# Optimization experiments

Measured on AMD Instinct MI355X. Metric: run time of the kernel, lower is better.

## Reference

```python
import jax, jax.numpy as jnp
import numpy as np

B, T, D, H = 2, 2048, 1024, 16
HS = D // H
EPS = 1e-5


def setup_inputs() -> dict:
    key = jax.random.key(0)
    ks = jax.random.split(key, 16)
    s = lambda *shape: 0.02
    inp = {
        "x": jax.random.normal(ks[0], (B, T, D), jnp.float32),
        # per-head Q/K/V weights stacked over heads: [H, D, HS]
        "Wq": jax.random.normal(ks[1], (H, D, HS), jnp.float32) * 0.02,
        "bq": jnp.zeros((H, HS), jnp.float32),
        "Wk": jax.random.normal(ks[2], (H, D, HS), jnp.float32) * 0.02,
        "bk": jnp.zeros((H, HS), jnp.float32),
        "Wv": jax.random.normal(ks[3], (H, D, HS), jnp.float32) * 0.02,
        "bv": jnp.zeros((H, HS), jnp.float32),
        "Wp": jax.random.normal(ks[4], (D, D), jnp.float32) * 0.02,
        "bp": jnp.zeros((D,), jnp.float32),
        "W1": jax.random.normal(ks[5], (D, 4 * D), jnp.float32) * 0.02,
        "b1": jnp.zeros((4 * D,), jnp.float32),
        "W2": jax.random.normal(ks[6], (4 * D, D), jnp.float32) * 0.02,
        "b2": jnp.zeros((D,), jnp.float32),
        "g1": jnp.ones((D,), jnp.float32),
        "be1": jnp.zeros((D,), jnp.float32),
        "g2": jnp.ones((D,), jnp.float32),
        "be2": jnp.zeros((D,), jnp.float32),
    }
    return inp


def layernorm(x, g, b):
    mu = jnp.mean(x, axis=-1, keepdims=True)
    var = jnp.mean(jnp.square(x - mu), axis=-1, keepdims=True)
    return (x - mu) * jax.lax.rsqrt(var + EPS) * g + b


def reference(x, Wq, bq, Wk, bk, Wv, bv, Wp, bp, W1, b1, W2, b2, g1, be1, g2, be2):
    # NOTE: this block applies LN then residual-adds the *normalized* x,
    # exactly as in the original (x = ln1(x); x = x + mha(x)).
    h = layernorm(x, g1, be1)
    # multi-head attention, all heads batched via stacked weights
    q = jnp.einsum('btd,hdk->bhtk', h, Wq) + bq[None, :, None, :]
    k = jnp.einsum('btd,hdk->bhtk', h, Wk) + bk[None, :, None, :]
    v = jnp.einsum('btd,hdk->bhtk', h, Wv) + bv[None, :, None, :]
    att = jnp.einsum('bhtk,bhsk->bhts', q, k) * (HS ** -0.5)  # [B,H,T,T]
    att = jax.nn.softmax(att, axis=-1)
    o = jnp.einsum('bhts,bhsk->bhtk', att, v)  # [B,H,T,HS]
    # concat heads in order along last dim -> [B,T,D]
    o = jnp.transpose(o, (0, 2, 1, 3)).reshape(B, T, D)
    o = o @ Wp + bp
    h = h + o
    h2 = layernorm(h, g2, be2)
    ff = jax.nn.gelu(h2 @ W1 + b1, approximate=False) @ W2 + b2
    return h2 + ff
```

## Files before the change

### kernel.cpp

```cpp
#include <hip/hip_runtime.h>
#include <cstdint>
#include <cstddef>

#define B_  2
#define T_  2048
#define D_  1024
#define H_  16
#define HS_ 64
#define MTOT (B_*T_)

typedef unsigned short u16;
typedef __attribute__((ext_vector_type(8))) __bf16 bf16x8;
typedef __attribute__((ext_vector_type(4))) float f32x4;

__device__ __forceinline__ u16 f2bf(float f) {
  unsigned int u = __builtin_bit_cast(unsigned int, f);
  u += 0x7fffu + ((u >> 16) & 1u);
  return (u16)(u >> 16);
}

__device__ __forceinline__ unsigned cvtpk(float lo, float hi) {
  unsigned r;
  asm("v_cvt_pk_bf16_f32 %0, %1, %2" : "=v"(r) : "v"(lo), "v"(hi));
  return r;
}

__device__ __forceinline__ void gload16(const u16* g, u16* l) {
  __builtin_amdgcn_global_load_lds((const __attribute__((address_space(1))) void*)g,
                                   (__attribute__((address_space(3))) void*)l, 16, 0, 0);
}

__global__ __launch_bounds__(256) void transpose_qkv(const float* __restrict__ wq,
                                                     const float* __restrict__ wk,
                                                     const float* __restrict__ wv,
                                                     u16* __restrict__ out) {
  __shared__ float tile[32][33];
  const int R = 1024, C = 64;
  int z = blockIdx.z, sel = z >> 4, zl = z & 15;
  const float* src = (sel == 0 ? wq : (sel == 1 ? wk : wv)) + (size_t)zl * R * C;
  u16* dst = out + (size_t)sel * 1024 * 1024 + (size_t)zl * R * C;
  int c0 = blockIdx.x * 32, r0 = blockIdx.y * 32;
  int tx = threadIdx.x & 31, ty = threadIdx.x >> 5;
#pragma unroll
  for (int k = 0; k < 4; ++k)
    tile[ty + k*8][tx] = src[(size_t)(r0 + ty + k*8) * C + c0 + tx];
  __syncthreads();
#pragma unroll
  for (int k = 0; k < 4; ++k)
    dst[(size_t)(c0 + ty + k*8) * R + r0 + tx] = f2bf(tile[tx][ty + k*8]);
}

__global__ __launch_bounds__(256) void transpose_f2b(const float* __restrict__ in,
                                                     u16* __restrict__ out, int R, int C) {
  __shared__ float tile[32][33];
  int c0 = blockIdx.x * 32, r0 = blockIdx.y * 32;
  size_t zoff = (size_t)blockIdx.z * R * C;
  const float* src = in + zoff;
  u16* dst = out + zoff;
  int tx = threadIdx.x & 31, ty = threadIdx.x >> 5;
#pragma unroll
  for (int k = 0; k < 4; ++k)
    tile[ty + k*8][tx] = src[(size_t)(r0 + ty + k*8) * C + c0 + tx];
  __syncthreads();
#pragma unroll
  for (int k = 0; k < 4; ++k)
    dst[(size_t)(c0 + ty + k*8) * R + r0 + tx] = f2bf(tile[tx][ty + k*8]);
}

__global__ __launch_bounds__(256) void transpose_v(const u16* __restrict__ in,
                                                   u16* __restrict__ out) {
  __shared__ u16 tile[32][33];
  int z = blockIdx.z;
  int b = z >> 4, h = z & 15;
  int t0 = blockIdx.x * 32, f0 = blockIdx.y * 32;
  int tx = threadIdx.x & 31, ty = threadIdx.x >> 5;
#pragma unroll
  for (int k = 0; k < 4; ++k)
    tile[ty + k*8][tx] = in[((size_t)b*T_ + t0 + ty + k*8) * D_ + h*HS_ + f0 + tx];
  __syncthreads();
#pragma unroll
  for (int k = 0; k < 4; ++k)
    out[((size_t)z*HS_ + f0 + ty + k*8) * T_ + t0 + tx] = tile[tx][ty + k*8];
}

__global__ __launch_bounds__(256) void ln_kernel(const float* __restrict__ x,
                                                 const float* __restrict__ gg,
                                                 const float* __restrict__ be,
                                                 float* __restrict__ hf,
                                                 u16* __restrict__ hb) {
  int row = blockIdx.x;
  int t = threadIdx.x;
  const float* xr = x + (size_t)row * D_;
  float4 xv = *(const float4*)&xr[t * 4];
  float s  = xv.x + xv.y + xv.z + xv.w;
  float ss = xv.x*xv.x + xv.y*xv.y + xv.z*xv.z + xv.w*xv.w;
#pragma unroll
  for (int m = 1; m < 64; m <<= 1) { s += __shfl_xor(s, m); ss += __shfl_xor(ss, m); }
  __shared__ float red[8];
  int lane = t & 63, wv = t >> 6;
  if (lane == 0) { red[wv] = s; red[4 + wv] = ss; }
  __syncthreads();
  s  = red[0] + red[1] + red[2] + red[3];
  ss = red[4] + red[5] + red[6] + red[7];
  float mu  = s * (1.0f / D_);
  float var = ss * (1.0f / D_) - mu * mu;
  float rs  = rsqrtf(var + 1e-5f);
  float4 gv = *(const float4*)&gg[t * 4];
  float4 bv = *(const float4*)&be[t * 4];
  float4 hv;
  hv.x = (xv.x - mu) * rs * gv.x + bv.x;
  hv.y = (xv.y - mu) * rs * gv.y + bv.y;
  hv.z = (xv.z - mu) * rs * gv.z + bv.z;
  hv.w = (xv.w - mu) * rs * gv.w + bv.w;
  *(float4*)&hf[(size_t)row * D_ + t * 4] = hv;
  uint2 pk;
  pk.x = (unsigned)f2bf(hv.x) | ((unsigned)f2bf(hv.y) << 16);
  pk.y = (unsigned)f2bf(hv.z) | ((unsigned)f2bf(hv.w) << 16);
  *(uint2*)&hb[(size_t)row * D_ + t * 4] = pk;
}

template<int EPI>
__global__ __launch_bounds__(512, 2) void gemm256(
    const u16* __restrict__ A, const u16* __restrict__ Bt,
    const float* __restrict__ bias0, const float* __restrict__ bias1,
    const float* __restrict__ bias2,
    u16* __restrict__ o0, u16* __restrict__ o1, u16* __restrict__ o2,
    int M, int N, int K) {
  __shared__ __align__(16) u16 As[2][256 * 64];
  __shared__ __align__(16) u16 Bs[2][256 * 64];
  const int tid = threadIdx.x;
  const int lane = tid & 63, w = tid >> 6;
  const int m0 = blockIdx.y * 256, n0 = blockIdx.x * 256;
  const int rA = lane & 15, g = lane >> 4;
  const int wm = (w >> 2) * 128, wn = (w & 3) * 64;
  const int sxa = rA & 7;

  f32x4 acc[8][4] = {};

  auto stage = [&](int t, int bufi) {
#pragma unroll
    for (int i = 0; i < 4; ++i) {
      int c = i * 512 + tid;
      int row = c >> 3;
      int ss = (c & 7) ^ (row & 7);
      gload16(A + (size_t)(m0 + row) * K + t * 64 + ss * 8,
              &As[bufi][0] + (size_t)(i * 512 + w * 64) * 8);
    }
#pragma unroll
    for (int i = 0; i < 4; ++i) {
      int c = i * 512 + tid;
      int row = c >> 3;
      int ss = (c & 7) ^ (row & 7);
      gload16(Bt + (size_t)(n0 + row) * K + t * 64 + ss * 8,
              &Bs[bufi][0] + (size_t)(i * 512 + w * 64) * 8);
    }
  };

  stage(0, 0);

  const int nk = K >> 6;
  for (int t = 0; t < nk; ++t) {
    __syncthreads();
    const int buf = t & 1;
    if (t + 1 < nk) stage(t + 1, buf ^ 1);

    bf16x8 bfr[4][2];
#pragma unroll
    for (int j = 0; j < 4; ++j) {
      int br = wn + j * 16 + rA;
#pragma unroll
      for (int kk = 0; kk < 2; ++kk)
        bfr[j][kk] = *(const bf16x8*)&Bs[buf][br * 64 + (((kk * 4 + g) ^ sxa) << 3)];
    }
#pragma unroll
    for (int i = 0; i < 8; ++i) {
      int ar = wm + i * 16 + rA;
      bf16x8 a0 = *(const bf16x8*)&As[buf][ar * 64 + ((g ^ sxa) << 3)];
      bf16x8 a1 = *(const bf16x8*)&As[buf][ar * 64 + (((4 + g) ^ sxa) << 3)];
#pragma unroll
      for (int j = 0; j < 4; ++j) {
        acc[i][j] = __builtin_amdgcn_mfma_f32_16x16x32_bf16(a0, bfr[j][0], acc[i][j], 0, 0, 0);
        acc[i][j] = __builtin_amdgcn_mfma_f32_16x16x32_bf16(a1, bfr[j][1], acc[i][j], 0, 0, 0);
      }
    }
  }

#pragma unroll
  for (int i = 0; i < 8; ++i) {
#pragma unroll
    for (int j = 0; j < 4; ++j) {
#pragma unroll
      for (int r = 0; r < 4; ++r) {
        int row = m0 + wm + i * 16 + g * 4 + r;
        int col = n0 + wn + j * 16 + rA;
        float v = acc[i][j][r];
        int sel = col >> 10, nn = col & 1023;
        const float* bp = sel == 0 ? bias0 : (sel == 1 ? bias1 : bias2);
        u16* op = sel == 0 ? o0 : (sel == 1 ? o1 : o2);
        op[(size_t)row * 1024 + nn] = f2bf(v + bp[nn]);
      }
    }
  }
}

template<int EPI>
__global__ __launch_bounds__(256) void gemm_bt(
    const u16* __restrict__ A, const u16* __restrict__ Bt,
    const float* __restrict__ bias0, const float* __restrict__ res,
    float* __restrict__ outf, float* __restrict__ p1, u16* __restrict__ ob,
    int M, int N, int K, int kLen) {
  __shared__ __align__(16) u16 As[3][128 * 32];
  __shared__ __align__(16) u16 Bs[3][128 * 32];
  const int tid = threadIdx.x;
  const int lane = tid & 63, wv = tid >> 6;
  const int m0 = blockIdx.y * 128, n0 = blockIdx.x * 128;
  const int kOff = blockIdx.z * kLen;
  const int rA = lane & 15, g = lane >> 4;
  const int wm = (wv >> 1) * 64, wn = (wv & 1) * 64;
  const int sx = (rA >> 1) & 3;

  f32x4 acc[4][4] = {};

  auto stage = [&](int tt, int bufi) {
#pragma unroll
    for (int p = 0; p < 2; ++p) {
      int c = (p * 4 + wv) * 64 + lane;
      int row = c >> 2;
      int s = (c & 3) ^ ((row >> 1) & 3);
      gload16(A  + (size_t)(m0 + row) * K + kOff + tt * 32 + s * 8,
              &As[bufi][0] + (size_t)(p * 4 + wv) * 512);
      gload16(Bt + (size_t)(n0 + row) * K + kOff + tt * 32 + s * 8,
              &Bs[bufi][0] + (size_t)(p * 4 + wv) * 512);
    }
  };

  const int nk = kLen >> 5;
  stage(0, 0);
  stage(1, 1);

  int cur = 0, nxt = 2;
  for (int t = 0; t < nk; ++t) {
    if (t + 1 < nk) asm volatile("s_waitcnt vmcnt(4)" ::: "memory");
    else            asm volatile("s_waitcnt vmcnt(0)" ::: "memory");
    __builtin_amdgcn_s_barrier();
    __builtin_amdgcn_sched_barrier(0);
    if (t + 2 < nk) stage(t + 2, nxt);

    bf16x8 a[4], b[4];
#pragma unroll
    for (int i = 0; i < 4; ++i)
      a[i] = *(const bf16x8*)&As[cur][(wm + i * 16 + rA) * 32 + ((g ^ sx) << 3)];
#pragma unroll
    for (int i = 0; i < 4; ++i)
      b[i] = *(const bf16x8*)&Bs[cur][(wn + i * 16 + rA) * 32 + ((g ^ sx) << 3)];
#pragma unroll
    for (int i = 0; i < 4; ++i)
#pragma unroll
      for (int j = 0; j < 4; ++j)
        acc[i][j] = __builtin_amdgcn_mfma_f32_16x16x32_bf16(a[i], b[j], acc[i][j], 0, 0, 0);

    cur = (cur == 2) ? 0 : cur + 1;
    nxt = (nxt == 2) ? 0 : nxt + 1;
  }

#pragma unroll
  for (int i = 0; i < 4; ++i) {
#pragma unroll
    for (int j = 0; j < 4; ++j) {
#pragma unroll
      for (int r = 0; r < 4; ++r) {
        int row = m0 + wm + i * 16 + g * 4 + r;
        int col = n0 + wn + j * 16 + rA;
        float v = acc[i][j][r];
        if constexpr (EPI == 1) {
          v += bias0[col];
          float z = 0.7978845608f * (v + 0.044715f * v * v * v);
          z = fminf(z, 18.0f);
          float e = __builtin_amdgcn_exp2f(z * 2.8853900817779268f);
          v = v * e / (e + 1.0f);
          ob[(size_t)row * N + col] = f2bf(v);
        } else if constexpr (EPI == 2) {
          v += bias0[col] + res[(size_t)row * N + col];
          outf[(size_t)row * N + col] = v;
        } else {
          float* dst = blockIdx.z ? p1 : outf;
          dst[(size_t)row * N + col] = v;
        }
      }
    }
  }
}

__global__ __launch_bounds__(256) void reduce_ff2(const float* __restrict__ p0,
                                                  const float* __restrict__ p1,
                                                  const float* __restrict__ bias,
                                                  const float* __restrict__ res,
                                                  float* __restrict__ out) {
  int i = (blockIdx.x * 256 + threadIdx.x) * 4;
  float4 a = *(const float4*)&p0[i];
  float4 b = *(const float4*)&p1[i];
  float4 r = *(const float4*)&res[i];
  float4 bb = *(const float4*)&bias[i & 1023];
  float4 o;
  o.x = a.x + b.x + r.x + bb.x;
  o.y = a.y + b.y + r.y + bb.y;
  o.z = a.z + b.z + r.z + bb.z;
  o.w = a.w + b.w + r.w + bb.w;
  *(float4*)&out[i] = o;
}

__global__ __launch_bounds__(256) void attn_kernel(const u16* __restrict__ qg,
                                                   const u16* __restrict__ kg,
                                                   const u16* __restrict__ vtg,
                                                   u16* __restrict__ og) {
  const int wg = blockIdx.x;
  const int qt = wg & 31;
  const int h  = (wg >> 5) & 15;
  const int b  = wg >> 9;
  const int tid = threadIdx.x, lane = tid & 63, wv = tid >> 6;
  const int q0 = qt * 64 + wv * 16;
  const int rA = lane & 15, g = lane >> 4;
  const int rx = rA & 7;

  __shared__ __align__(16) u16 Ks[2][64 * 64];
  __shared__ __align__(16) u16 Vs[2][64 * 64];
  __shared__ __align__(16) u16 Ps[4][16 * 64];

  const size_t qoff = ((size_t)b * T_ + q0 + rA) * D_ + h * HS_ + g * 8;
  const bf16x8 aq0 = *(const bf16x8*)&qg[qoff];
  const bf16x8 aq1 = *(const bf16x8*)&qg[qoff + 32];

  const u16* kbase = kg + (size_t)b * T_ * D_ + h * HS_;
  const u16* vbase = vtg + ((size_t)b * H_ + h) * HS_ * T_;

  const float cfold = 0.18033688011112042f;
  float mrun = -1e30f, lrun = 0.0f;
  f32x4 oacc[4] = {};

  auto stage = [&](int t, int buf) {
#pragma unroll
    for (int p = 0; p < 2; ++p) {
      int chunk = p * 256 + wv * 64 + lane;
      int row = chunk >> 3, s = chunk & 7;
      int ss = s ^ (row & 7);
      gload16(kbase + ((size_t)t * 64 + row) * D_ + ss * 8,
              &Ks[buf][0] + (size_t)(p * 256 + wv * 64) * 8);
      gload16(vbase + (size_t)row * T_ + t * 64 + ss * 8,
              &Vs[buf][0] + (size_t)(p * 256 + wv * 64) * 8);
    }
  };

  stage(0, 0);

  const int NT = T_ / 64;
  for (int t = 0; t < NT; ++t) {
    __syncthreads();
    const int buf = t & 1;
    if (t + 1 < NT) stage(t + 1, buf ^ 1);

    const u16* kb = &Ks[buf][0];
    f32x4 sc[4];
    __builtin_amdgcn_s_setprio(1);
#pragma unroll
    for (int st = 0; st < 4; ++st) {
      bf16x8 k0 = *(const bf16x8*)&kb[(st * 16 + rA) * 64 + ((g ^ rx) << 3)];
      bf16x8 k1 = *(const bf16x8*)&kb[(st * 16 + rA) * 64 + (((4 + g) ^ rx) << 3)];
      f32x4 z = {};
      z = __builtin_amdgcn_mfma_f32_16x16x32_bf16(k0, aq0, z, 0, 0, 0);
      z = __builtin_amdgcn_mfma_f32_16x16x32_bf16(k1, aq1, z, 0, 0, 0);
      sc[st] = z;
    }
    __builtin_amdgcn_s_setprio(0);

    float a0 = fmaxf(fmaxf(sc[0][0], sc[0][1]), fmaxf(sc[0][2], sc[0][3]));
    float a1 = fmaxf(fmaxf(sc[1][0], sc[1][1]), fmaxf(sc[1][2], sc[1][3]));
    float a2 = fmaxf(fmaxf(sc[2][0], sc[2][1]), fmaxf(sc[2][2], sc[2][3]));
    float a3 = fmaxf(fmaxf(sc[3][0], sc[3][1]), fmaxf(sc[3][2], sc[3][3]));
    float mx = fmaxf(fmaxf(a0, a1), fmaxf(a2, a3));
    mx = fmaxf(mx, __shfl_xor(mx, 16));
    mx = fmaxf(mx, __shfl_xor(mx, 32));
    float tm = mx * cfold;

    if (__any(tm > mrun + 8.0f)) {
      float mnew = fmaxf(mrun, tm);
      float sca = __builtin_amdgcn_exp2f(mrun - mnew);
      mrun = mnew;
      lrun *= sca;
#pragma unroll
      for (int f = 0; f < 4; ++f) oacc[f] *= sca;
    }

    float p[16];
#pragma unroll
    for (int st = 0; st < 4; ++st)
#pragma unroll
      for (int r = 0; r < 4; ++r)
        p[st * 4 + r] = __builtin_amdgcn_exp2f(__builtin_fmaf(sc[st][r], cfold, -mrun));

    float sum = (((p[0] + p[1]) + (p[2] + p[3])) + ((p[4] + p[5]) + (p[6] + p[7])))
              + (((p[8] + p[9]) + (p[10] + p[11])) + ((p[12] + p[13]) + (p[14] + p[15])));
    sum += __shfl_xor(sum, 16);
    sum += __shfl_xor(sum, 32);
    lrun += sum;

    char* psb = (char*)&Ps[wv][0];
#pragma unroll
    for (int st = 0; st < 4; ++st) {
      uint2 w;
      w.x = cvtpk(p[st * 4 + 0], p[st * 4 + 1]);
      w.y = cvtpk(p[st * 4 + 2], p[st * 4 + 3]);
      int slot = st * 2 + (g >> 1);
      *(uint2*)&psb[rA * 128 + (((slot ^ rx)) << 4) + ((g & 1) << 3)] = w;
    }
    bf16x8 pf0 = *(const bf16x8*)&psb[rA * 128 + ((g ^ rx) << 4)];
    bf16x8 pf1 = *(const bf16x8*)&psb[rA * 128 + (((4 + g) ^ rx) << 4)];

    const u16* vbl = &Vs[buf][0];
    __builtin_amdgcn_s_setprio(1);
#pragma unroll
    for (int f = 0; f < 4; ++f) {
      bf16x8 v0 = *(const bf16x8*)&vbl[(f * 16 + rA) * 64 + ((g ^ rx) << 3)];
      bf16x8 v1 = *(const bf16x8*)&vbl[(f * 16 + rA) * 64 + (((4 + g) ^ rx) << 3)];
      oacc[f] = __builtin_amdgcn_mfma_f32_16x16x32_bf16(v0, pf0, oacc[f], 0, 0, 0);
      oacc[f] = __builtin_amdgcn_mfma_f32_16x16x32_bf16(v1, pf1, oacc[f], 0, 0, 0);
    }
    __builtin_amdgcn_s_setprio(0);
  }

  float linv = 1.0f / lrun;
#pragma unroll
  for (int f = 0; f < 4; ++f) {
    uint2 w;
    w.x = cvtpk(oacc[f][0] * linv, oacc[f][1] * linv);
    w.y = cvtpk(oacc[f][2] * linv, oacc[f][3] * linv);
    *(uint2*)&og[((size_t)b * T_ + q0 + rA) * D_ + h * HS_ + f * 16 + g * 4] = w;
  }
}

extern "C" void kernel_launch(void* const* d_in, const int* in_sizes, int n_in,
                              void* d_out, int out_size, void* d_ws, size_t ws_size,
                              hipStream_t stream) {
  const float* x   = (const float*)d_in[0];
  const float* Wq  = (const float*)d_in[1];
  const float* bq  = (const float*)d_in[2];
  const float* Wk  = (const float*)d_in[3];
  const float* bk  = (const float*)d_in[4];
  const float* Wv  = (const float*)d_in[5];
  const float* bv  = (const float*)d_in[6];
  const float* Wp  = (const float*)d_in[7];
  const float* bp  = (const float*)d_in[8];
  const float* W1  = (const float*)d_in[9];
  const float* b1  = (const float*)d_in[10];
  const float* W2  = (const float*)d_in[11];
  const float* b2  = (const float*)d_in[12];
  const float* g1  = (const float*)d_in[13];
  const float* be1 = (const float*)d_in[14];
  const float* g2  = (const float*)d_in[15];
  const float* be2 = (const float*)d_in[16];
  float* out = (float*)d_out;

  char* w = (char*)d_ws;
  auto alloc = [&](size_t bytes) { char* p = w; w += (bytes + 255) & ~(size_t)255; return p; };
  const size_t MD = (size_t)MTOT * D_;

  float* h_f    = (float*)alloc(MD * 4);
  u16*   h_b    = (u16*)  alloc(MD * 2);
  u16*   wqkv_t = (u16*)  alloc(3 * (size_t)D_ * D_ * 2);
  u16*   wp_t   = (u16*)  alloc((size_t)D_ * D_ * 2);
  u16*   w1_t   = (u16*)  alloc((size_t)D_ * 4 * D_ * 2);
  u16*   w2_t   = (u16*)  alloc((size_t)D_ * 4 * D_ * 2);
  u16*   q_b    = (u16*)  alloc(MD * 2);
  u16*   k_b    = (u16*)  alloc(MD * 2);
  u16*   v_b    = (u16*)  alloc(MD * 2);
  u16*   vt_b   = (u16*)  alloc(MD * 2);
  u16*   o_b    = (u16*)  alloc(MD * 2);
  float* hat_f  = (float*)alloc(MD * 4);
  u16*   ff1_b  = q_b;
  float* h2_f   = h_f;
  u16*   h2_b   = h_b;
  float* pf0    = hat_f;
  float* pf1    = (float*)h_b;

  dim3 blk(256);

  transpose_qkv<<<dim3(2, 32, 48), blk, 0, stream>>>(Wq, Wk, Wv, wqkv_t);
  transpose_f2b<<<dim3(32, 32, 1), blk, 0, stream>>>(Wp, wp_t, 1024, 1024);
  transpose_f2b<<<dim3(128, 32, 1), blk, 0, stream>>>(W1, w1_t, 1024, 4096);
  transpose_f2b<<<dim3(32, 128, 1), blk, 0, stream>>>(W2, w2_t, 4096, 1024);

  ln_kernel<<<dim3(MTOT), blk, 0, stream>>>(x, g1, be1, h_f, h_b);

  gemm256<0><<<dim3(12, 16), dim3(512), 0, stream>>>(h_b, wqkv_t, bq, bk, bv,
      q_b, k_b, v_b, MTOT, 3072, 1024);

  transpose_v<<<dim3(64, 2, 32), blk, 0, stream>>>(v_b, vt_b);

  attn_kernel<<<dim3(B_ * H_ * (T_ / 64)), blk, 0, stream>>>(q_b, k_b, vt_b, o_b);

  gemm_bt<2><<<dim3(8, 32, 1), blk, 0, stream>>>(o_b, wp_t, bp, h_f, hat_f,
      nullptr, nullptr, MTOT, 1024, 1024, 1024);

  ln_kernel<<<dim3(MTOT), blk, 0, stream>>>(hat_f, g2, be2, h2_f, h2_b);

  gemm_bt<1><<<dim3(32, 32, 1), blk, 0, stream>>>(h2_b, w1_t, b1, nullptr,
      nullptr, nullptr, ff1_b, MTOT, 4096, 1024, 1024);

  gemm_bt<3><<<dim3(8, 32, 2), blk, 0, stream>>>(ff1_b, w2_t, nullptr, nullptr,
      pf0, pf1, nullptr, MTOT, 1024, 4096, 2048);

  reduce_ff2<<<dim3(MTOT), blk, 0, stream>>>(pf0, pf1, b2, h2_f, out);
}
```

Measured before the change: 286.3 us.

## Fuse V transpose into QKV epilogue, merge weight transposes, narrow proj GEMM tile

The QKV GEMM epilogue now writes V straight into the transposed [B,H,HS,T] layout as packed bf16 pairs, so the separate transpose_v kernel and its round trip through global memory go away. The three fp32-to-bf16 weight transpose launches are merged into one kernel with a flat grid. The output-projection GEMM gets a TN template parameter and runs with 128x64 tiles, doubling its block count to 512 for better CU occupancy. The V stores are 8-byte writes strided by T, so they are less coalesced than the row-major stores.

Measured after the change: 279.6 us. -2.3%, faster.

```diff
diff --git a/kernel.cpp b/kernel.cpp
--- a/kernel.cpp
+++ b/kernel.cpp
@@ -50,13 +50,17 @@
     dst[(size_t)(c0 + ty + k*8) * R + r0 + tx] = f2bf(tile[tx][ty + k*8]);
 }
 
-__global__ __launch_bounds__(256) void transpose_f2b(const float* __restrict__ in,
-                                                     u16* __restrict__ out, int R, int C) {
+__global__ __launch_bounds__(256) void transpose_rest(
+    const float* __restrict__ Wp, const float* __restrict__ W1,
+    const float* __restrict__ W2, u16* __restrict__ wp_t,
+    u16* __restrict__ w1_t, u16* __restrict__ w2_t) {
   __shared__ float tile[32][33];
-  int c0 = blockIdx.x * 32, r0 = blockIdx.y * 32;
-  size_t zoff = (size_t)blockIdx.z * R * C;
-  const float* src = in + zoff;
-  u16* dst = out + zoff;
+  int f = blockIdx.x;
+  const float* src; u16* dst; int R, C, xx, yy;
+  if (f < 1024)      { src = Wp; dst = wp_t; R = 1024; C = 1024; xx = f & 31;  yy = f >> 5; }
+  else if (f < 5120) { int f2 = f - 1024; src = W1; dst = w1_t; R = 1024; C = 4096; xx = f2 & 127; yy = f2 >> 7; }
+  else               { int f2 = f - 5120; src = W2; dst = w2_t; R = 4096; C = 1024; xx = f2 & 31;  yy = f2 >> 5; }
+  int c0 = xx * 32, r0 = yy * 32;
   int tx = threadIdx.x & 31, ty = threadIdx.x >> 5;
 #pragma unroll
   for (int k = 0; k < 4; ++k)
@@ -65,22 +69,6 @@
 #pragma unroll
   for (int k = 0; k < 4; ++k)
     dst[(size_t)(c0 + ty + k*8) * R + r0 + tx] = f2bf(tile[tx][ty + k*8]);
-}
-
-__global__ __launch_bounds__(256) void transpose_v(const u16* __restrict__ in,
-                                                   u16* __restrict__ out) {
-  __shared__ u16 tile[32][33];
-  int z = blockIdx.z;
-  int b = z >> 4, h = z & 15;
-  int t0 = blockIdx.x * 32, f0 = blockIdx.y * 32;
-  int tx = threadIdx.x & 31, ty = threadIdx.x >> 5;
-#pragma unroll
-  for (int k = 0; k < 4; ++k)
-    tile[ty + k*8][tx] = in[((size_t)b*T_ + t0 + ty + k*8) * D_ + h*HS_ + f0 + tx];
-  __syncthreads();
-#pragma unroll
-  for (int k = 0; k < 4; ++k)
-    out[((size_t)z*HS_ + f0 + ty + k*8) * T_ + t0 + tx] = tile[tx][ty + k*8];
 }
 
 __global__ __launch_bounds__(256) void ln_kernel(const float* __restrict__ x,
@@ -189,37 +177,45 @@
   for (int i = 0; i < 8; ++i) {
 #pragma unroll
     for (int j = 0; j < 4; ++j) {
-#pragma unroll
-      for (int r = 0; r < 4; ++r) {
-        int row = m0 + wm + i * 16 + g * 4 + r;
-        int col = n0 + wn + j * 16 + rA;
-        float v = acc[i][j][r];
-        int sel = col >> 10, nn = col & 1023;
-        const float* bp = sel == 0 ? bias0 : (sel == 1 ? bias1 : bias2);
-        u16* op = sel == 0 ? o0 : (sel == 1 ? o1 : o2);
-        op[(size_t)row * 1024 + nn] = f2bf(v + bp[nn]);
+      int col = n0 + wn + j * 16 + rA;
+      int sel = col >> 10, nn = col & 1023;
+      int row0 = m0 + wm + i * 16 + g * 4;
+      if (sel == 2) {
+        float bb = bias2[nn];
+        int bb_ = row0 >> 11, t0 = row0 & 2047;
+        uint2 pkv;
+        pkv.x = cvtpk(acc[i][j][0] + bb, acc[i][j][1] + bb);
+        pkv.y = cvtpk(acc[i][j][2] + bb, acc[i][j][3] + bb);
+        *(uint2*)&o2[((size_t)(bb_ * 1024 + nn)) * 2048 + t0] = pkv;
+      } else {
+        const float* bp = sel == 0 ? bias0 : bias1;
+        u16* op = sel == 0 ? o0 : o1;
+#pragma unroll
+        for (int r = 0; r < 4; ++r)
+          op[(size_t)(row0 + r) * 1024 + nn] = f2bf(acc[i][j][r] + bp[nn]);
       }
     }
   }
 }
 
-template<int EPI>
+template<int EPI, int TN>
 __global__ __launch_bounds__(256) void gemm_bt(
     const u16* __restrict__ A, const u16* __restrict__ Bt,
     const float* __restrict__ bias0, const float* __restrict__ res,
     float* __restrict__ outf, float* __restrict__ p1, u16* __restrict__ ob,
     int M, int N, int K, int kLen) {
+  constexpr int NJ = TN / 32;
   __shared__ __align__(16) u16 As[3][128 * 32];
-  __shared__ __align__(16) u16 Bs[3][128 * 32];
+  __shared__ __align__(16) u16 Bs[3][TN * 32];
   const int tid = threadIdx.x;
   const int lane = tid & 63, wv = tid >> 6;
-  const int m0 = blockIdx.y * 128, n0 = blockIdx.x * 128;
+  const int m0 = blockIdx.y * 128, n0 = blockIdx.x * TN;
   const int kOff = blockIdx.z * kLen;
   const int rA = lane & 15, g = lane >> 4;
-  const int wm = (wv >> 1) * 64, wn = (wv & 1) * 64;
+  const int wm = (wv >> 1) * 64, wn = (wv & 1) * (TN / 2);
   const int sx = (rA >> 1) & 3;
 
-  f32x4 acc[4][4] = {};
+  f32x4 acc[4][NJ] = {};
 
   auto stage = [&](int tt, int bufi) {
 #pragma unroll
@@ -227,8 +223,14 @@
       int c = (p * 4 + wv) * 64 + lane;
       int row = c >> 2;
       int s = (c & 3) ^ ((row >> 1) & 3);
-      gload16(A  + (size_t)(m0 + row) * K + kOff + tt * 32 + s * 8,
+      gload16(A + (size_t)(m0 + row) * K + kOff + tt * 32 + s * 8,
               &As[bufi][0] + (size_t)(p * 4 + wv) * 512);
+    }
+#pragma unroll
+    for (int p = 0; p < TN / 64; ++p) {
+      int c = (p * 4 + wv) * 64 + lane;
+      int row = c >> 2;
+      int s = (c & 3) ^ ((row >> 1) & 3);
       gload16(Bt + (size_t)(n0 + row) * K + kOff + tt * 32 + s * 8,
               &Bs[bufi][0] + (size_t)(p * 4 + wv) * 512);
     }
@@ -246,17 +248,17 @@
     __builtin_amdgcn_sched_barrier(0);
     if (t + 2 < nk) stage(t + 2, nxt);
 
-    bf16x8 a[4], b[4];
+    bf16x8 a[4], b[NJ];
 #pragma unroll
     for (int i = 0; i < 4; ++i)
       a[i] = *(const bf16x8*)&As[cur][(wm + i * 16 + rA) * 32 + ((g ^ sx) << 3)];
 #pragma unroll
+    for (int j = 0; j < NJ; ++j)
+      b[j] = *(const bf16x8*)&Bs[cur][(wn + j * 16 + rA) * 32 + ((g ^ sx) << 3)];
+#pragma unroll
     for (int i = 0; i < 4; ++i)
-      b[i] = *(const bf16x8*)&Bs[cur][(wn + i * 16 + rA) * 32 + ((g ^ sx) << 3)];
-#pragma unroll
-    for (int i = 0; i < 4; ++i)
-#pragma unroll
-      for (int j = 0; j < 4; ++j)
+#pragma unroll
+      for (int j = 0; j < NJ; ++j)
         acc[i][j] = __builtin_amdgcn_mfma_f32_16x16x32_bf16(a[i], b[j], acc[i][j], 0, 0, 0);
 
     cur = (cur == 2) ? 0 : cur + 1;
@@ -266,7 +268,7 @@
 #pragma unroll
   for (int i = 0; i < 4; ++i) {
 #pragma unroll
-    for (int j = 0; j < 4; ++j) {
+    for (int j = 0; j < NJ; ++j) {
 #pragma unroll
       for (int r = 0; r < 4; ++r) {
         int row = m0 + wm + i * 16 + g * 4 + r;
@@ -480,32 +482,29 @@
   u16*   h2_b   = h_b;
   float* pf0    = hat_f;
   float* pf1    = (float*)h_b;
+  (void)v_b;
 
   dim3 blk(256);
 
   transpose_qkv<<<dim3(2, 32, 48), blk, 0, stream>>>(Wq, Wk, Wv, wqkv_t);
-  transpose_f2b<<<dim3(32, 32, 1), blk, 0, stream>>>(Wp, wp_t, 1024, 1024);
-  transpose_f2b<<<dim3(128, 32, 1), blk, 0, stream>>>(W1, w1_t, 1024, 4096);
-  transpose_f2b<<<dim3(32, 128, 1), blk, 0, stream>>>(W2, w2_t, 4096, 1024);
+  transpose_rest<<<dim3(9216), blk, 0, stream>>>(Wp, W1, W2, wp_t, w1_t, w2_t);
 
   ln_kernel<<<dim3(MTOT), blk, 0, stream>>>(x, g1, be1, h_f, h_b);
 
   gemm256<0><<<dim3(12, 16), dim3(512), 0, stream>>>(h_b, wqkv_t, bq, bk, bv,
-      q_b, k_b, v_b, MTOT, 3072, 1024);
-
-  transpose_v<<<dim3(64, 2, 32), blk, 0, stream>>>(v_b, vt_b);
+      q_b, k_b, vt_b, MTOT, 3072, 1024);
 
   attn_kernel<<<dim3(B_ * H_ * (T_ / 64)), blk, 0, stream>>>(q_b, k_b, vt_b, o_b);
 
-  gemm_bt<2><<<dim3(8, 32, 1), blk, 0, stream>>>(o_b, wp_t, bp, h_f, hat_f,
+  gemm_bt<2, 64><<<dim3(16, 32, 1), blk, 0, stream>>>(o_b, wp_t, bp, h_f, hat_f,
       nullptr, nullptr, MTOT, 1024, 1024, 1024);
 
   ln_kernel<<<dim3(MTOT), blk, 0, stream>>>(hat_f, g2, be2, h2_f, h2_b);
 
-  gemm_bt<1><<<dim3(32, 32, 1), blk, 0, stream>>>(h2_b, w1_t, b1, nullptr,
+  gemm_bt<1, 128><<<dim3(32, 32, 1), blk, 0, stream>>>(h2_b, w1_t, b1, nullptr,
       nullptr, nullptr, ff1_b, MTOT, 4096, 1024, 1024);
 
-  gemm_bt<3><<<dim3(8, 32, 2), blk, 0, stream>>>(ff1_b, w2_t, nullptr, nullptr,
+  gemm_bt<3, 128><<<dim3(8, 32, 2), blk, 0, stream>>>(ff1_b, w2_t, nullptr, nullptr,
       pf0, pf1, nullptr, MTOT, 1024, 4096, 2048);
 
   reduce_ff2<<<dim3(MTOT), blk, 0, stream>>>(pf0, pf1, b2, h2_f, out);
```
